# Performance work log

Hardware: AMD Instinct MI355X
Metric: run time of the kernel (lower is better)

## Reference

```python
import jax, jax.numpy as jnp
import numpy as np

HID = 10     # hidden_size
IN = 4       # input_size
OUT = 4
P = 5        # predict_ahead


def setup_inputs() -> dict:
    key = jax.random.key(0)
    ks = jax.random.split(key, 7)
    B, T = 16384, 100
    x = jax.random.normal(ks[0], (B, T, IN), dtype=jnp.float32)
    s = 1.0 / np.sqrt(HID)  # PyTorch default uniform init bound
    W_ih = jax.random.uniform(ks[1], (4 * HID, IN), jnp.float32, -s, s)
    W_hh = jax.random.uniform(ks[2], (4 * HID, HID), jnp.float32, -s, s)
    b_ih = jax.random.uniform(ks[3], (4 * HID,), jnp.float32, -s, s)
    b_hh = jax.random.uniform(ks[4], (4 * HID,), jnp.float32, -s, s)
    W_lin = jax.random.uniform(ks[5], (OUT, HID), jnp.float32, -s, s)
    b_lin = jax.random.uniform(ks[6], (OUT,), jnp.float32, -s, s)
    return {"x": x, "W_ih": W_ih, "W_hh": W_hh, "b_ih": b_ih,
            "b_hh": b_hh, "W_lin": W_lin, "b_lin": b_lin}


def _lstm_cell(xt, h, c, W_ih, W_hh, b_ih, b_hh):
    # PyTorch gate order: i, f, g, o
    gates = xt @ W_ih.T + h @ W_hh.T + (b_ih + b_hh)  # [B, 4H]
    i, f, g, o = jnp.split(gates, 4, axis=-1)
    c_new = jax.nn.sigmoid(f) * c + jax.nn.sigmoid(i) * jnp.tanh(g)
    h_new = jax.nn.sigmoid(o) * jnp.tanh(c_new)
    return h_new, c_new


def reference(x, W_ih, W_hh, b_ih, b_hh, W_lin, b_lin):
    B, T, _ = x.shape
    Tp = T - P + 1  # number of outer time steps
    h0 = jnp.zeros((B, HID), x.dtype)
    c0 = jnp.zeros((B, HID), x.dtype)
    xs = jnp.transpose(x[:, :Tp, :], (1, 0, 2))  # [Tp, B, IN]

    def step(carry, xt):
        h, c = carry
        h, c = _lstm_cell(xt, h, c, W_ih, W_hh, b_ih, b_hh)
        y = h @ W_lin.T + b_lin  # [B, OUT]
        outs = [y]
        h_a, c_a = h, c
        for _ in range(P - 1):
            h_a, c_a = _lstm_cell(y, h_a, c_a, W_ih, W_hh, b_ih, b_hh)
            y = h_a @ W_lin.T + b_lin
            outs.append(y)
        return (h, c), jnp.stack(outs, axis=1)  # [B, P, OUT]

    (h, c), ys = jax.lax.scan(step, (h0, c0), xs)  # ys: [Tp, B, P, OUT]
    final_output = jnp.transpose(ys, (1, 0, 2, 3))  # [B, Tp, P, OUT]
    return final_output, c[None]  # c_t: [num_layers=1, B, HID]
```

## Files before the change

### kernel.cpp

```cpp
#include <hip/hip_runtime.h>


#define HIDN 10
#define INPN 4
#define OUTN 4
#define PN   5
#define TN   100
#define TPN  96
#define BN   16384
#define GPB  24

typedef float v2f __attribute__((ext_vector_type(2)));

#define PIN(x) asm volatile("" : "+v"(x))

__device__ __forceinline__ float rcpf_(float v) { return __builtin_amdgcn_rcpf(v); }
__device__ __forceinline__ float e2_(float v)   { return __builtin_amdgcn_exp2f(v); }
__device__ __forceinline__ float sig2_(float g)  { return rcpf_(1.0f + e2_(-g)); }
__device__ __forceinline__ float tanh2_(float g) { return fmaf(-2.0f, rcpf_(1.0f + e2_(g)), 1.0f); }

#define K2L2E 2.88539008177792681472f

__global__ __launch_bounds__(256, 3) void lstm_ar_kernel(
    const float* __restrict__ x,
    const float* __restrict__ W_ih,
    const float* __restrict__ W_hh,
    const float* __restrict__ b_ih,
    const float* __restrict__ b_hh,
    const float* __restrict__ W_lin,
    const float* __restrict__ b_lin,
    float* __restrict__ out)
{
    __shared__ __align__(16) float s_h[GPB][PN][20];
    __shared__ __align__(16) float s_y[GPB][4];

    const int tid = threadIdx.x;
    const int wid = tid >> 6;
    const int wl  = tid & 63;
    const int grp = wl / 10;
    const int u   = wl - grp * 10;
    const int slot  = wid * 6 + grp;
    const int batch = blockIdx.x * GPB + slot;
    if (grp >= 6 || batch >= BN) return;

    const float L2E = 1.44269504088896340736f;
    const float rs[4] = { L2E, L2E, 2.0f * L2E, L2E };

    v2f  wc2[4][5];
    v2f  wih2[4][2];
    v2f  br2[4];
    #pragma unroll
    for (int r = 0; r < 4; ++r) {
        const int j = u + r * 10;
        float wihr[INPN];
        #pragma unroll
        for (int q = 0; q < INPN; ++q) wihr[q] = W_ih[j * INPN + q];
        float brr = b_ih[j] + b_hh[j];
        #pragma unroll
        for (int q = 0; q < INPN; ++q) brr += wihr[q] * b_lin[q];
        #pragma unroll
        for (int k = 0; k < HIDN; ++k) {
            float wck = W_hh[j * HIDN + k];
            #pragma unroll
            for (int q = 0; q < INPN; ++q) wck += wihr[q] * W_lin[q * HIDN + k];
            if (k & 1) wc2[r][k >> 1].y = wck * rs[r];
            else       wc2[r][k >> 1].x = wck * rs[r];
        }
        #pragma unroll
        for (int q = 0; q < INPN; ++q) {
            if (q & 1) wih2[r][q >> 1].y = wihr[q] * rs[r];
            else       wih2[r][q >> 1].x = wihr[q] * rs[r];
        }
        br2[r] = v2f{ brr * rs[r], 0.0f };
    }

    const int pmine = u >> 1;
    const int opair = (u & 1) * 2;
    v2f yl0[5], yl1[5];
    #pragma unroll
    for (int k = 0; k < HIDN; k += 2) {
        yl0[k >> 1] = v2f{ W_lin[opair * HIDN + k],        W_lin[opair * HIDN + k + 1] };
        yl1[k >> 1] = v2f{ W_lin[(opair + 1) * HIDN + k],  W_lin[(opair + 1) * HIDN + k + 1] };
    }
    v2f ybv0 = v2f{ b_lin[opair],     0.0f };
    v2f ybv1 = v2f{ b_lin[opair + 1], 0.0f };

    #pragma unroll
    for (int r = 0; r < 4; ++r) {
        #pragma unroll
        for (int k = 0; k < 5; ++k) PIN(wc2[r][k]);
        PIN(wih2[r][0]); PIN(wih2[r][1]); PIN(br2[r]);
    }
    #pragma unroll
    for (int k = 0; k < 5; ++k) { PIN(yl0[k]); PIN(yl1[k]); }
    PIN(ybv0); PIN(ybv1);

    s_h[slot][0][u] = 0.0f;
    if (u < 4) s_y[slot][u] = b_lin[u];
    __builtin_amdgcn_wave_barrier();

    const float* xb   = x + (long)batch * TN * INPN;
    float*       outb = out + (long)batch * TPN * PN * OUTN;

    float cm = 0.0f;
    float4 xcur = *(const float4*)xb;
    for (int t = 0; t < TPN; ++t) {
        float4 xnext = *(const float4*)(xb + (t + 1) * INPN);

        v2f h2[5];
        float g[4];

        {
            float4 yp = *(const float4*)&s_y[slot][0];
            float4 a  = *(const float4*)&s_h[slot][0][0];
            float4 b  = *(const float4*)&s_h[slot][0][4];
            float2 c2 = *(const float2*)&s_h[slot][0][8];
            h2[0] = v2f{a.x, a.y}; h2[1] = v2f{a.z, a.w};
            h2[2] = v2f{b.x, b.y}; h2[3] = v2f{b.z, b.w};
            h2[4] = v2f{c2.x, c2.y};
            v2f dxa = v2f{xcur.x - yp.x, xcur.y - yp.y};
            v2f dxc = v2f{xcur.z - yp.z, xcur.w - yp.w};
            #pragma unroll
            for (int r = 0; r < 4; ++r) {
                v2f acc = br2[r];
                acc = __builtin_elementwise_fma(wih2[r][0], dxa, acc);
                acc = __builtin_elementwise_fma(wih2[r][1], dxc, acc);
                #pragma unroll
                for (int k = 0; k < 5; ++k)
                    acc = __builtin_elementwise_fma(wc2[r][k], h2[k], acc);
                g[r] = acc.x + acc.y;
            }
            float iv = sig2_(g[0]), fv = sig2_(g[1]), gv = tanh2_(g[2]), ov = sig2_(g[3]);
            cm = fmaf(fv, cm, iv * gv);
            float hn = ov * tanh2_(cm * K2L2E);
            s_h[slot][0][u] = hn;
        }
        __builtin_amdgcn_wave_barrier();

        float cr = cm;
        #pragma unroll
        for (int p = 1; p < PN; ++p) {
            float4 a  = *(const float4*)&s_h[slot][p - 1][0];
            float4 b  = *(const float4*)&s_h[slot][p - 1][4];
            float2 c2 = *(const float2*)&s_h[slot][p - 1][8];
            h2[0] = v2f{a.x, a.y}; h2[1] = v2f{a.z, a.w};
            h2[2] = v2f{b.x, b.y}; h2[3] = v2f{b.z, b.w};
            h2[4] = v2f{c2.x, c2.y};
            #pragma unroll
            for (int r = 0; r < 4; ++r) {
                v2f acc = br2[r];
                #pragma unroll
                for (int k = 0; k < 5; ++k)
                    acc = __builtin_elementwise_fma(wc2[r][k], h2[k], acc);
                g[r] = acc.x + acc.y;
            }
            float iv = sig2_(g[0]), fv = sig2_(g[1]), gv = tanh2_(g[2]), ov = sig2_(g[3]);
            cr = fmaf(fv, cr, iv * gv);
            float hn = ov * tanh2_(cr * K2L2E);
            s_h[slot][p][u] = hn;
            __builtin_amdgcn_wave_barrier();
        }

        {
            float4 a  = *(const float4*)&s_h[slot][pmine][0];
            float4 b  = *(const float4*)&s_h[slot][pmine][4];
            float2 c2 = *(const float2*)&s_h[slot][pmine][8];
            v2f h0 = v2f{a.x, a.y},  h1 = v2f{a.z, a.w};
            v2f h3 = v2f{b.x, b.y},  h4 = v2f{b.z, b.w};
            v2f h5 = v2f{c2.x, c2.y};
            v2f a0 = ybv0, a1 = ybv1;
            a0 = __builtin_elementwise_fma(yl0[0], h0, a0);
            a1 = __builtin_elementwise_fma(yl1[0], h0, a1);
            a0 = __builtin_elementwise_fma(yl0[1], h1, a0);
            a1 = __builtin_elementwise_fma(yl1[1], h1, a1);
            a0 = __builtin_elementwise_fma(yl0[2], h3, a0);
            a1 = __builtin_elementwise_fma(yl1[2], h3, a1);
            a0 = __builtin_elementwise_fma(yl0[3], h4, a0);
            a1 = __builtin_elementwise_fma(yl1[3], h4, a1);
            a0 = __builtin_elementwise_fma(yl0[4], h5, a0);
            a1 = __builtin_elementwise_fma(yl1[4], h5, a1);
            float2 yv; yv.x = a0.x + a0.y; yv.y = a1.x + a1.y;
            *(float2*)(outb + t * PN * OUTN + 2 * u) = yv;
            if (u < 2) *(float2*)&s_y[slot][2 * u] = yv;
        }
        __builtin_amdgcn_wave_barrier();

        xcur = xnext;
    }

    out[(long)BN * TPN * PN * OUTN + (long)batch * HIDN + u] = cm;
}

extern "C" void kernel_launch(void* const* d_in, const int* in_sizes, int n_in,
                              void* d_out, int out_size, void* d_ws, size_t ws_size,
                              hipStream_t stream) {
    const float* x     = (const float*)d_in[0];
    const float* W_ih  = (const float*)d_in[1];
    const float* W_hh  = (const float*)d_in[2];
    const float* b_ih  = (const float*)d_in[3];
    const float* b_hh  = (const float*)d_in[4];
    const float* W_lin = (const float*)d_in[5];
    const float* b_lin = (const float*)d_in[6];
    float* out = (float*)d_out;

    const int grid = (BN + GPB - 1) / GPB;
    lstm_ar_kernel<<<grid, 256, 0, stream>>>(x, W_ih, W_hh, b_ih, b_hh, W_lin, b_lin, out);
}
```

Baseline: 185.7 us.

## Decouple main LSTM recurrence from rollout and software-pipeline them

The main-step recurrence now uses the raw W_hh and the true input x instead of the previous prediction, so it no longer depends on the rollout output y. The next main step is computed before the previous step's autoregressive rollout, and the two are interleaved to expose instruction-level parallelism. LDS is double-buffered for the main hidden state. The extra weight set raises register pressure, so the occupancy hint drops from 3 to 2 blocks per CU.

Result: slower. 192.2 us (+3.5%).

```diff
diff --git a/kernel.cpp b/kernel.cpp
--- a/kernel.cpp
+++ b/kernel.cpp
@@ -21,7 +21,7 @@
 
 #define K2L2E 2.88539008177792681472f
 
-__global__ __launch_bounds__(256, 3) void lstm_ar_kernel(
+__global__ __launch_bounds__(256, 2) void lstm_ar_kernel(
     const float* __restrict__ x,
     const float* __restrict__ W_ih,
     const float* __restrict__ W_hh,
@@ -31,8 +31,7 @@
     const float* __restrict__ b_lin,
     float* __restrict__ out)
 {
-    __shared__ __align__(16) float s_h[GPB][PN][20];
-    __shared__ __align__(16) float s_y[GPB][4];
+    __shared__ __align__(16) float s_h[GPB][6][20];
 
     const int tid = threadIdx.x;
     const int wid = tid >> 6;
@@ -46,8 +45,10 @@
     const float L2E = 1.44269504088896340736f;
     const float rs[4] = { L2E, L2E, 2.0f * L2E, L2E };
 
+    v2f  wm2[4][5];
     v2f  wc2[4][5];
     v2f  wih2[4][2];
+    v2f  bm2[4];
     v2f  br2[4];
     #pragma unroll
     for (int r = 0; r < 4; ++r) {
@@ -55,22 +56,25 @@
         float wihr[INPN];
         #pragma unroll
         for (int q = 0; q < INPN; ++q) wihr[q] = W_ih[j * INPN + q];
-        float brr = b_ih[j] + b_hh[j];
+        float bmr = b_ih[j] + b_hh[j];
+        float brr = bmr;
         #pragma unroll
         for (int q = 0; q < INPN; ++q) brr += wihr[q] * b_lin[q];
         #pragma unroll
         for (int k = 0; k < HIDN; ++k) {
-            float wck = W_hh[j * HIDN + k];
+            float wmk = W_hh[j * HIDN + k];
+            float wck = wmk;
             #pragma unroll
             for (int q = 0; q < INPN; ++q) wck += wihr[q] * W_lin[q * HIDN + k];
-            if (k & 1) wc2[r][k >> 1].y = wck * rs[r];
-            else       wc2[r][k >> 1].x = wck * rs[r];
+            if (k & 1) { wm2[r][k >> 1].y = wmk * rs[r]; wc2[r][k >> 1].y = wck * rs[r]; }
+            else       { wm2[r][k >> 1].x = wmk * rs[r]; wc2[r][k >> 1].x = wck * rs[r]; }
         }
         #pragma unroll
         for (int q = 0; q < INPN; ++q) {
             if (q & 1) wih2[r][q >> 1].y = wihr[q] * rs[r];
             else       wih2[r][q >> 1].x = wihr[q] * rs[r];
         }
+        bm2[r] = v2f{ bmr * rs[r], 0.0f };
         br2[r] = v2f{ brr * rs[r], 0.0f };
     }
 
@@ -79,8 +83,8 @@
     v2f yl0[5], yl1[5];
     #pragma unroll
     for (int k = 0; k < HIDN; k += 2) {
-        yl0[k >> 1] = v2f{ W_lin[opair * HIDN + k],        W_lin[opair * HIDN + k + 1] };
-        yl1[k >> 1] = v2f{ W_lin[(opair + 1) * HIDN + k],  W_lin[(opair + 1) * HIDN + k + 1] };
+        yl0[k >> 1] = v2f{ W_lin[opair * HIDN + k],       W_lin[opair * HIDN + k + 1] };
+        yl1[k >> 1] = v2f{ W_lin[(opair + 1) * HIDN + k], W_lin[(opair + 1) * HIDN + k + 1] };
     }
     v2f ybv0 = v2f{ b_lin[opair],     0.0f };
     v2f ybv1 = v2f{ b_lin[opair + 1], 0.0f };
@@ -88,105 +92,108 @@
     #pragma unroll
     for (int r = 0; r < 4; ++r) {
         #pragma unroll
-        for (int k = 0; k < 5; ++k) PIN(wc2[r][k]);
-        PIN(wih2[r][0]); PIN(wih2[r][1]); PIN(br2[r]);
+        for (int k = 0; k < 5; ++k) { PIN(wm2[r][k]); PIN(wc2[r][k]); }
+        PIN(wih2[r][0]); PIN(wih2[r][1]); PIN(bm2[r]); PIN(br2[r]);
     }
     #pragma unroll
     for (int k = 0; k < 5; ++k) { PIN(yl0[k]); PIN(yl1[k]); }
     PIN(ybv0); PIN(ybv1);
 
-    s_h[slot][0][u] = 0.0f;
-    if (u < 4) s_y[slot][u] = b_lin[u];
-    __builtin_amdgcn_wave_barrier();
-
     const float* xb   = x + (long)batch * TN * INPN;
     float*       outb = out + (long)batch * TPN * PN * OUTN;
 
     float cm = 0.0f;
-    float4 xcur = *(const float4*)xb;
-    for (int t = 0; t < TPN; ++t) {
-        float4 xnext = *(const float4*)(xb + (t + 1) * INPN);
-
-        v2f h2[5];
+    v2f h2m[5], h2n[5];
+    #pragma unroll
+    for (int k = 0; k < 5; ++k) h2m[k] = v2f{0.0f, 0.0f};
+
+    auto CELL = [&](const float g[4], float& c) -> float {
+        float iv = sig2_(g[0]), fv = sig2_(g[1]), gv = tanh2_(g[2]), ov = sig2_(g[3]);
+        c = fmaf(fv, c, iv * gv);
+        return ov * tanh2_(c * K2L2E);
+    };
+
+    auto MAIN = [&](int t, float4 xv) {
+        v2f xa = v2f{xv.x, xv.y}, xc = v2f{xv.z, xv.w};
         float g[4];
-
-        {
-            float4 yp = *(const float4*)&s_y[slot][0];
-            float4 a  = *(const float4*)&s_h[slot][0][0];
-            float4 b  = *(const float4*)&s_h[slot][0][4];
-            float2 c2 = *(const float2*)&s_h[slot][0][8];
-            h2[0] = v2f{a.x, a.y}; h2[1] = v2f{a.z, a.w};
-            h2[2] = v2f{b.x, b.y}; h2[3] = v2f{b.z, b.w};
-            h2[4] = v2f{c2.x, c2.y};
-            v2f dxa = v2f{xcur.x - yp.x, xcur.y - yp.y};
-            v2f dxc = v2f{xcur.z - yp.z, xcur.w - yp.w};
+        #pragma unroll
+        for (int r = 0; r < 4; ++r) {
+            v2f acc = bm2[r];
+            acc = __builtin_elementwise_fma(wih2[r][0], xa, acc);
+            acc = __builtin_elementwise_fma(wih2[r][1], xc, acc);
             #pragma unroll
-            for (int r = 0; r < 4; ++r) {
-                v2f acc = br2[r];
-                acc = __builtin_elementwise_fma(wih2[r][0], dxa, acc);
-                acc = __builtin_elementwise_fma(wih2[r][1], dxc, acc);
-                #pragma unroll
-                for (int k = 0; k < 5; ++k)
-                    acc = __builtin_elementwise_fma(wc2[r][k], h2[k], acc);
-                g[r] = acc.x + acc.y;
-            }
-            float iv = sig2_(g[0]), fv = sig2_(g[1]), gv = tanh2_(g[2]), ov = sig2_(g[3]);
-            cm = fmaf(fv, cm, iv * gv);
-            float hn = ov * tanh2_(cm * K2L2E);
-            s_h[slot][0][u] = hn;
-        }
+            for (int k = 0; k < 5; ++k)
+                acc = __builtin_elementwise_fma(wm2[r][k], h2m[k], acc);
+            g[r] = acc.x + acc.y;
+        }
+        float hn = CELL(g, cm);
+        s_h[slot][t & 1][u] = hn;
         __builtin_amdgcn_wave_barrier();
-
-        float cr = cm;
+        const v2f* hp = (const v2f*)&s_h[slot][t & 1][0];
+        #pragma unroll
+        for (int k = 0; k < 5; ++k) h2n[k] = hp[k];
+    };
+
+    auto ROLLOUT = [&](int tt, float cro) {
+        v2f hr2[5];
+        #pragma unroll
+        for (int k = 0; k < 5; ++k) hr2[k] = h2m[k];
+        float cr = cro;
+        float g[4];
         #pragma unroll
         for (int p = 1; p < PN; ++p) {
-            float4 a  = *(const float4*)&s_h[slot][p - 1][0];
-            float4 b  = *(const float4*)&s_h[slot][p - 1][4];
-            float2 c2 = *(const float2*)&s_h[slot][p - 1][8];
-            h2[0] = v2f{a.x, a.y}; h2[1] = v2f{a.z, a.w};
-            h2[2] = v2f{b.x, b.y}; h2[3] = v2f{b.z, b.w};
-            h2[4] = v2f{c2.x, c2.y};
             #pragma unroll
             for (int r = 0; r < 4; ++r) {
                 v2f acc = br2[r];
                 #pragma unroll
                 for (int k = 0; k < 5; ++k)
-                    acc = __builtin_elementwise_fma(wc2[r][k], h2[k], acc);
+                    acc = __builtin_elementwise_fma(wc2[r][k], hr2[k], acc);
                 g[r] = acc.x + acc.y;
             }
-            float iv = sig2_(g[0]), fv = sig2_(g[1]), gv = tanh2_(g[2]), ov = sig2_(g[3]);
-            cr = fmaf(fv, cr, iv * gv);
-            float hn = ov * tanh2_(cr * K2L2E);
-            s_h[slot][p][u] = hn;
+            float hn = CELL(g, cr);
+            s_h[slot][1 + p][u] = hn;
             __builtin_amdgcn_wave_barrier();
-        }
-
-        {
-            float4 a  = *(const float4*)&s_h[slot][pmine][0];
-            float4 b  = *(const float4*)&s_h[slot][pmine][4];
-            float2 c2 = *(const float2*)&s_h[slot][pmine][8];
-            v2f h0 = v2f{a.x, a.y},  h1 = v2f{a.z, a.w};
-            v2f h3 = v2f{b.x, b.y},  h4 = v2f{b.z, b.w};
-            v2f h5 = v2f{c2.x, c2.y};
-            v2f a0 = ybv0, a1 = ybv1;
-            a0 = __builtin_elementwise_fma(yl0[0], h0, a0);
-            a1 = __builtin_elementwise_fma(yl1[0], h0, a1);
-            a0 = __builtin_elementwise_fma(yl0[1], h1, a0);
-            a1 = __builtin_elementwise_fma(yl1[1], h1, a1);
-            a0 = __builtin_elementwise_fma(yl0[2], h3, a0);
-            a1 = __builtin_elementwise_fma(yl1[2], h3, a1);
-            a0 = __builtin_elementwise_fma(yl0[3], h4, a0);
-            a1 = __builtin_elementwise_fma(yl1[3], h4, a1);
-            a0 = __builtin_elementwise_fma(yl0[4], h5, a0);
-            a1 = __builtin_elementwise_fma(yl1[4], h5, a1);
-            float2 yv; yv.x = a0.x + a0.y; yv.y = a1.x + a1.y;
-            *(float2*)(outb + t * PN * OUTN + 2 * u) = yv;
-            if (u < 2) *(float2*)&s_y[slot][2 * u] = yv;
-        }
-        __builtin_amdgcn_wave_barrier();
-
+            if (p < PN - 1) {
+                const v2f* hp = (const v2f*)&s_h[slot][1 + p][0];
+                #pragma unroll
+                for (int k = 0; k < 5; ++k) hr2[k] = hp[k];
+            }
+        }
+        const int rowy = (pmine == 0) ? (tt & 1) : (pmine + 1);
+        const v2f* hq = (const v2f*)&s_h[slot][rowy][0];
+        v2f h0 = hq[0], h1 = hq[1], h3 = hq[2], h4 = hq[3], h5 = hq[4];
+        v2f a0 = ybv0, a1 = ybv1;
+        a0 = __builtin_elementwise_fma(yl0[0], h0, a0);
+        a1 = __builtin_elementwise_fma(yl1[0], h0, a1);
+        a0 = __builtin_elementwise_fma(yl0[1], h1, a0);
+        a1 = __builtin_elementwise_fma(yl1[1], h1, a1);
+        a0 = __builtin_elementwise_fma(yl0[2], h3, a0);
+        a1 = __builtin_elementwise_fma(yl1[2], h3, a1);
+        a0 = __builtin_elementwise_fma(yl0[3], h4, a0);
+        a1 = __builtin_elementwise_fma(yl1[3], h4, a1);
+        a0 = __builtin_elementwise_fma(yl0[4], h5, a0);
+        a1 = __builtin_elementwise_fma(yl1[4], h5, a1);
+        float2 yv; yv.x = a0.x + a0.y; yv.y = a1.x + a1.y;
+        *(float2*)(outb + tt * PN * OUTN + 2 * u) = yv;
+    };
+
+    float4 xcur = *(const float4*)xb;
+    MAIN(0, xcur);
+    xcur = *(const float4*)(xb + INPN);
+
+    for (int t = 1; t < TPN; ++t) {
+        float4 xnext = *(const float4*)(xb + (t + 1) * INPN);
+        #pragma unroll
+        for (int k = 0; k < 5; ++k) h2m[k] = h2n[k];
+        float cro = cm;
+        MAIN(t, xcur);
+        ROLLOUT(t - 1, cro);
         xcur = xnext;
     }
+
+    #pragma unroll
+    for (int k = 0; k < 5; ++k) h2m[k] = h2n[k];
+    ROLLOUT(TPN - 1, cm);
 
     out[(long)BN * TPN * PN * OUTN + (long)batch * HIDN + u] = cm;
 }
```
